# Kernel optimization log

Hardware: AMD Instinct MI355X
Metric: run time of the kernel (lower is better)

The kernel has to match this reference:

```python
import jax, jax.numpy as jnp
import numpy as np

N_STATE = 512
M_IN = 64
P_OUT = 64
BATCH = 32
SEQ = 2048


def setup_inputs() -> dict:
    key = jax.random.key(0)
    k1, k2, k3, k4, k5 = jax.random.split(key, 5)
    u = jax.random.normal(k1, (BATCH, SEQ, M_IN), dtype=jnp.float32)
    # CompanionParam init: a ~ randn * 0.01 (keeps companion matrix stable, near shift matrix)
    a = jax.random.normal(k2, (N_STATE,), dtype=jnp.float32) * 0.01
    B = jax.random.normal(k3, (N_STATE, M_IN), dtype=jnp.float32) * 0.05
    C = jax.random.normal(k4, (P_OUT, N_STATE), dtype=jnp.float32) * 0.05
    D = jax.random.normal(k5, (P_OUT, M_IN), dtype=jnp.float32) * 0.05
    return {"u": u, "a": a, "B": B, "C": C, "D": D}


def companion_matrix(a):
    # A[i+1, i] = 1 on subdiagonal; last column = -flip(a)  (matches CompanionParam.matrix)
    n = a.shape[0]
    idx = jnp.arange(n - 1)
    A = jnp.zeros((n, n), dtype=a.dtype)
    A = A.at[idx + 1, idx].set(1.0)
    A = A.at[:, n - 1].set(-a[::-1])
    return A


def reference(u, a, B, C, D):
    # LTI SSM recurrence: x_t = A x_{t-1} + B u_t ; y_t = C x_t + D u_t
    A = companion_matrix(a)  # (n, n)
    batch, T, m = u.shape
    n = a.shape[0]
    u_t = jnp.transpose(u, (1, 0, 2))  # (T, batch, m)
    Bu = jnp.einsum('tbm,nm->tbn', u_t, B)  # precompute input drive (T, batch, n)

    def step(x, bu):
        x_new = x @ A.T + bu  # (batch, n)
        return x_new, x_new

    x0 = jnp.zeros((batch, n), dtype=u.dtype)
    _, xs = jax.lax.scan(step, x0, Bu)  # xs: (T, batch, n)
    ys = jnp.einsum('tbn,pn->tbp', xs, C) + jnp.einsum('tbm,pm->tbp', u_t, D)
    return jnp.transpose(ys, (1, 0, 2))  # (batch, T, p)
```

## Files before the change

### kernel.cpp

```cpp
#include <hip/hip_runtime.h>

#define SEQ  2048
#define NB   32
#define NS   512
#define MI   64
#define PO   64
#define TB   64
#define NTB  32
#define CH   64
#define NCH  8
#define LDU  72
#define LDD  68
#define SG_LDA 72

typedef __attribute__((ext_vector_type(8))) __bf16 bf16x8;
typedef __attribute__((ext_vector_type(4))) float  floatx4;

__device__ inline unsigned short f2bf(float f) {
    unsigned u = __builtin_bit_cast(unsigned, f);
    u += 0x7fff + ((u >> 16) & 1);
    return (unsigned short)(u >> 16);
}

__global__ void __launch_bounds__(1024) prep_all_kernel(
    const float* __restrict__ u, const float* __restrict__ B,
    const float* __restrict__ C, const float* __restrict__ D,
    const float* __restrict__ a,
    unsigned short* __restrict__ ubf, unsigned short* __restrict__ BflatT,
    unsigned short* __restrict__ Bws, unsigned short* __restrict__ Cws,
    unsigned short* __restrict__ Dws, unsigned short* __restrict__ qT,
    float* __restrict__ hbuf) {
    __shared__ __align__(16) char smem[24576];
    const int bx = blockIdx.x, tid = threadIdx.x;
    if (bx < 512) {
        const size_t base = ((size_t)bx * 1024 + tid) * 8;
        float4 f0 = *(const float4*)(u + base);
        float4 f1 = *(const float4*)(u + base + 4);
        unsigned short tmp[8];
        tmp[0] = f2bf(f0.x); tmp[1] = f2bf(f0.y); tmp[2] = f2bf(f0.z); tmp[3] = f2bf(f0.w);
        tmp[4] = f2bf(f1.x); tmp[5] = f2bf(f1.y); tmp[6] = f2bf(f1.z); tmp[7] = f2bf(f1.w);
        *(uint4*)(ubf + base) = *(uint4*)&tmp[0];
    } else if (bx < 768) {
        const int i = (bx - 512) * 2 + (tid >> 9);
        const int id = tid & 511;
        const int j = id >> 3, q8 = (id & 7) * 8;
        unsigned short tmp[8];
        if (i >= j) {
            const float4 f0 = *(const float4*)(B + (size_t)(i - j) * MI + q8);
            const float4 f1 = *(const float4*)(B + (size_t)(i - j) * MI + q8 + 4);
            tmp[0] = f2bf(f0.x); tmp[1] = f2bf(f0.y); tmp[2] = f2bf(f0.z); tmp[3] = f2bf(f0.w);
            tmp[4] = f2bf(f1.x); tmp[5] = f2bf(f1.y); tmp[6] = f2bf(f1.z); tmp[7] = f2bf(f1.w);
        } else {
#pragma unroll
            for (int z = 0; z < 8; ++z) tmp[z] = 0;
        }
        *(uint4*)(BflatT + (size_t)i * 4096 + j * 64 + q8) = *(uint4*)&tmp[0];
    } else if (bx < 800) {
        float* a_ext = (float*)smem;
        const int p = (bx - 768) * 2 + (tid >> 9);
        const int j0 = tid & 511;
        a_ext[tid] = (tid < NS) ? a[tid] : 0.f;
        __syncthreads();
        float acc0 = 0.f;
        const float4* crow = (const float4*)(C + (size_t)p * NS);
        for (int i4 = 0; i4 < NS / 4; ++i4) {
            const float4 cv = crow[i4];
            const int base = 511 - i4 * 4;
            acc0 += cv.x * a_ext[base + j0]     + cv.y * a_ext[base - 1 + j0] +
                    cv.z * a_ext[base - 2 + j0] + cv.w * a_ext[base - 3 + j0];
        }
        qT[(size_t)p * NS + j0] = f2bf(acc0);
    } else if (bx < 868) {
        const int idx = (bx - 800) * 1024 + tid;
        const int nB = NS * MI, nC = PO * NS, nD = PO * MI;
        if (idx < nB) Bws[idx] = f2bf(B[idx]);
        else if (idx < nB + nC) Cws[idx - nB] = f2bf(C[idx - nB]);
        else if (idx < nB + nC + nD) Dws[idx - nB - nC] = f2bf(D[idx - nB - nC]);
    } else {
        float* a_l     = (float*)smem;
        float* h_ext   = (float*)(smem + 2560);
        float* part    = (float*)(smem + 12800);
        float* rhs_ext = (float*)(smem + 20992);
        const int kk = tid & 63, grp = tid >> 6;

        for (int x = tid; x < 640; x += 1024) a_l[x] = (x < NS) ? a[x] : 0.f;
        for (int x = tid; x < 640; x += 1024) h_ext[x] = 0.f;
        if (tid < 256) rhs_ext[tid] = 0.f;
        __syncthreads();

        float aw[34];
#pragma unroll
        for (int i = 0; i < 34; ++i) aw[i] = a_l[2 * kk + grp * 32 + i];

        if (tid < 64) {
            if (tid == 0) h_ext[512] = 1.f;
            float acc = (tid >= 1) ? a_l[tid - 1] : 0.f;
            for (int s = 1; s < 64; ++s) {
                const float hs = -__shfl(acc, s);
                if (tid == s) h_ext[512 + s] = hs;
                const float av = a_l[(tid > s) ? (tid - 1 - s) : 0];
                acc += (tid > s) ? av * hs : 0.f;
            }
        }
        __syncthreads();

        int t0 = 64;
        while (t0 < SEQ) {
            float acc0 = 0.f, acc1 = 0.f;
#pragma unroll
            for (int m = 0; m < 8; ++m) {
                const float4 hv = *(const float4*)&h_ext[512 + t0 - grp * 32 - 4 - 4 * m];
                acc0 += aw[4 * m + 0] * hv.w + aw[4 * m + 1] * hv.z +
                        aw[4 * m + 2] * hv.y + aw[4 * m + 3] * hv.x;
                acc1 += aw[4 * m + 1] * hv.w + aw[4 * m + 2] * hv.z +
                        aw[4 * m + 3] * hv.y + aw[4 * m + 4] * hv.x;
            }
            *(float2*)&part[grp * 128 + 2 * kk] = make_float2(acc0, acc1);
            __syncthreads();
            if (tid < 128) {
                float r = 0.f;
#pragma unroll
                for (int g = 0; g < 16; ++g) r += part[g * 128 + tid];
                rhs_ext[128 + tid] = -r;
            }
            __syncthreads();
            {
                const int g = tid >> 7, out = tid & 127;
                const int k0 = g * 16;
                float s = 0.f;
#pragma unroll
                for (int k4 = 0; k4 < 4; ++k4) {
                    const float4 h4 = *(const float4*)&h_ext[512 + k0 + 4 * k4];
                    const int base = 128 + out - k0 - 4 * k4;
                    s += h4.x * rhs_ext[base]     + h4.y * rhs_ext[base - 1] +
                         h4.z * rhs_ext[base - 2] + h4.w * rhs_ext[base - 3];
                }
                part[g * 128 + out] = s;
            }
            __syncthreads();
            if (tid < 128) {
                float r = 0.f;
#pragma unroll
                for (int g = 0; g < 8; ++g) r += part[g * 128 + tid];
                h_ext[512 + t0 + tid] = r;
            }
            __syncthreads();
            t0 += (t0 == 64) ? 64 : 128;
        }
        for (int i = tid; i < SEQ; i += 1024) hbuf[i] = h_ext[512 + i];
    }
}

__global__ void __launch_bounds__(256) sgemm_kernel(const unsigned short* __restrict__ ubf,
                                                    const unsigned short* __restrict__ BflatT,
                                                    float* __restrict__ Sbuf) {
    __shared__ unsigned short A_l[2][4 * 64 * SG_LDA];
    __shared__ unsigned short U_l[2][4 * 32 * SG_LDA];
    const int ib = blockIdx.x, b = blockIdx.y;
    const int tid = threadIdx.x, lane = tid & 63, w = tid >> 6;
    const int row16 = lane & 15, quad = lane >> 4;
    const int i0 = ib * 64;
    floatx4 acc[2];
#pragma unroll
    for (int ns = 0; ns < 2; ++ns) acc[ns] = (floatx4){0.f, 0.f, 0.f, 0.f};

    auto stage = [&](int jg, int buf) {
#pragma unroll
        for (int r = 0; r < 8; ++r) {
            const int id = tid + r * 256;
            const int row = id >> 5;
            const int jj = (id >> 3) & 3, q8 = (id & 7) * 8;
            const int j = jg * 4 + jj;
            *(uint4*)&A_l[buf][(jj * 64 + row) * SG_LDA + q8] =
                *(const uint4*)(BflatT + (size_t)(i0 + row) * 4096 + j * 64 + q8);
        }
#pragma unroll
        for (int r = 0; r < 4; ++r) {
            const int id = tid + r * 256;
            const int n = id >> 5;
            const int jj = (id >> 3) & 3, q8 = (id & 7) * 8;
            const int j = jg * 4 + jj;
            *(uint4*)&U_l[buf][(jj * 32 + n) * SG_LDA + q8] =
                *(const uint4*)(ubf + ((size_t)b * SEQ + n * 64 + 63 - j) * MI + q8);
        }
    };

    stage(0, 0);
    __syncthreads();
    for (int jg = 0; jg < 16; ++jg) {
        const int cur = jg & 1;
        if (jg + 1 < 16) stage(jg + 1, cur ^ 1);
#pragma unroll
        for (int jj = 0; jj < 4; ++jj) {
#pragma unroll
            for (int mk = 0; mk < 2; ++mk) {
                const bf16x8 av = *(const bf16x8*)
                    &A_l[cur][(jj * 64 + w * 16 + row16) * SG_LDA + mk * 32 + quad * 8];
#pragma unroll
                for (int ns = 0; ns < 2; ++ns) {
                    const bf16x8 bv = *(const bf16x8*)
                        &U_l[cur][(jj * 32 + ns * 16 + row16) * SG_LDA + mk * 32 + quad * 8];
                    acc[ns] = __builtin_amdgcn_mfma_f32_16x16x32_bf16(av, bv, acc[ns], 0, 0, 0);
                }
            }
        }
        __syncthreads();
    }
#pragma unroll
    for (int ns = 0; ns < 2; ++ns) {
        const int n = ns * 16 + row16;
        float* dst = Sbuf + ((size_t)b * NTB + n) * NS + i0 + w * 16 + quad * 4;
        *(floatx4*)dst = acc[ns];
    }
}

__global__ void __launch_bounds__(256, 4) ytile_kernel(
    const unsigned short* __restrict__ ubf, const unsigned short* __restrict__ Bws,
    const unsigned short* __restrict__ Cws, const unsigned short* __restrict__ Dws,
    const float* __restrict__ Sbuf, float* __restrict__ fbuf, float* __restrict__ y) {
    __shared__ __align__(16) float buDiag[TB * LDD];
    __shared__ __align__(16) unsigned short Gb[TB * LDU];
    __shared__ float seedL[NS];

    const int blk = blockIdx.x, b = blockIdx.y;
    const int t0 = blk * TB;
    const int tid = threadIdx.x;
    const int lane = tid & 63, w = tid >> 6;
    const int row16 = lane & 15, quad = lane >> 4;

    const int dd = lane >> 2, seg = lane & 3;
    const int d  = w * 16 + dd;
    const int tsplit = 63 - d, gseg = tsplit >> 4, jsplit = tsplit & 15;
    const int qb = lane & 60;

    {
        const int mtop = (blk - 1 < 7) ? (blk - 1) : 7;
#pragma unroll
        for (int half = 0; half < 2; ++half) {
            const int s = tid + half * 256;
            const int i = s - 1, q = i >> 6, r = i & 63;
            const int mmax = (mtop < q) ? mtop : q;
            float sd = 0.f;
#pragma unroll
            for (int m = 0; m < 8; ++m) {
                const bool ok = (m <= mmax);
                long off = ((long)b * NTB + (blk - 1 - m)) * NS + (q - m) * 64 + r;
                off = (off < 0) ? 0 : off;
                const float v = Sbuf[off];
                sd += ok ? v : 0.f;
            }
            seedL[s] = sd;
        }
    }

    float cB = 0.f;

    floatx4 accY[4];
#pragma unroll
    for (int nt = 0; nt < 4; ++nt) accY[nt] = (floatx4){0.f, 0.f, 0.f, 0.f};

    bf16x8 ufr0[4], ufr1[4];
#pragma unroll
    for (int nt = 0; nt < 4; ++nt) {
        const size_t ub = ((size_t)b * SEQ + t0 + nt * 16 + row16) * MI;
        ufr0[nt] = *(const bf16x8*)(ubf + ub + quad * 8);
        ufr1[nt] = *(const bf16x8*)(ubf + ub + 32 + quad * 8);
    }

    for (int ch = 0; ch < NCH; ++ch) {
        const bf16x8 bf0 = *(const bf16x8*)(Bws + (size_t)(ch * CH + w * 16 + row16) * MI + quad * 8);
        const bf16x8 bf1 = *(const bf16x8*)(Bws + (size_t)(ch * CH + w * 16 + row16) * MI + 32 + quad * 8);
        const bf16x8 cf0 = *(const bf16x8*)(Cws + (size_t)(w * 16 + row16) * NS + ch * CH + quad * 8);
        const bf16x8 cf1 = *(const bf16x8*)(Cws + (size_t)(w * 16 + row16) * NS + ch * CH + 32 + quad * 8);

#pragma unroll
        for (int nt = 0; nt < 4; ++nt) {
            floatx4 dacc = {0.f, 0.f, 0.f, 0.f};
            dacc = __builtin_amdgcn_mfma_f32_16x16x32_bf16(bf0, ufr0[nt], dacc, 0, 0, 0);
            dacc = __builtin_amdgcn_mfma_f32_16x16x32_bf16(bf1, ufr1[nt], dacc, 0, 0, 0);
            const int t = nt * 16 + row16;
            const int ibase = w * 16 + quad * 4;
#pragma unroll
            for (int r = 0; r < 4; ++r) {
                const int dscat = (ibase + r - t) & 63;
                buDiag[dscat * LDD + t] = dacc[r];
            }
        }
        __syncthreads();

        {
            const float sA = seedL[ch * CH + d];
            const float* rowp = &buDiag[d * LDD + seg * 16];
            const float4 v0 = *(const float4*)(rowp + 0);
            const float4 v1 = *(const float4*)(rowp + 4);
            const float4 v2 = *(const float4*)(rowp + 8);
            const float4 v3 = *(const float4*)(rowp + 12);
            float pv[16];
            pv[0]  = v0.x;          pv[1]  = pv[0]  + v0.y;
            pv[2]  = pv[1]  + v0.z; pv[3]  = pv[2]  + v0.w;
            pv[4]  = pv[3]  + v1.x; pv[5]  = pv[4]  + v1.y;
            pv[6]  = pv[5]  + v1.z; pv[7]  = pv[6]  + v1.w;
            pv[8]  = pv[7]  + v2.x; pv[9]  = pv[8]  + v2.y;
            pv[10] = pv[9]  + v2.z; pv[11] = pv[10] + v2.w;
            pv[12] = pv[11] + v3.x; pv[13] = pv[12] + v3.y;
            pv[14] = pv[13] + v3.z; pv[15] = pv[14] + v3.w;
            const float total = pv[15];
            const float tq0 = __shfl(total, qb + 0);
            const float tq1 = __shfl(total, qb + 1);
            const float tq2 = __shfl(total, qb + 2);
            const float off = (seg > 0 ? tq0 : 0.f) + (seg > 1 ? tq1 : 0.f) +
                              (seg > 2 ? tq2 : 0.f);
            float plocal = pv[0];
#pragma unroll
            for (int j = 1; j < 16; ++j) plocal = (j == jsplit) ? pv[j] : plocal;
            const float Ps = __shfl(off + plocal, qb + gseg);
            const float exitv = sA + Ps;
            const float baseLo = sA, baseHi = cB - Ps;
#pragma unroll
            for (int j = 0; j < 16; ++j) {
                const int t = seg * 16 + j;
                const float outv = ((t <= tsplit) ? baseLo : baseHi) + off + pv[j];
                Gb[t * LDU + ((d + t) & 63)] = f2bf(outv);
            }
            if (ch == NCH - 1) {
                if (seg == 0) fbuf[(size_t)b * SEQ + t0 + tsplit] = exitv;
            }
            cB = exitv;
        }
        __syncthreads();

#pragma unroll
        for (int nt = 0; nt < 4; ++nt) {
            const int t = nt * 16 + row16;
            bf16x8 g0 = *(const bf16x8*)&Gb[t * LDU + quad * 8];
            bf16x8 g1 = *(const bf16x8*)&Gb[t * LDU + 32 + quad * 8];
            accY[nt] = __builtin_amdgcn_mfma_f32_16x16x32_bf16(cf0, g0, accY[nt], 0, 0, 0);
            accY[nt] = __builtin_amdgcn_mfma_f32_16x16x32_bf16(cf1, g1, accY[nt], 0, 0, 0);
        }
    }

    const bf16x8 df0 = *(const bf16x8*)(Dws + (size_t)(w * 16 + row16) * MI + quad * 8);
    const bf16x8 df1 = *(const bf16x8*)(Dws + (size_t)(w * 16 + row16) * MI + 32 + quad * 8);
#pragma unroll
    for (int nt = 0; nt < 4; ++nt) {
        const int t = nt * 16 + row16;
        accY[nt] = __builtin_amdgcn_mfma_f32_16x16x32_bf16(df0, ufr0[nt], accY[nt], 0, 0, 0);
        accY[nt] = __builtin_amdgcn_mfma_f32_16x16x32_bf16(df1, ufr1[nt], accY[nt], 0, 0, 0);
        const int p0 = w * 16 + quad * 4;
        *(floatx4*)(y + ((size_t)b * SEQ + t0 + t) * PO + p0) = accY[nt];
    }
}

__global__ void __launch_bounds__(256) sconv_kernel(const float* __restrict__ fbuf,
                                                    const float* __restrict__ hbuf,
                                                    unsigned short* __restrict__ sbuf) {
    __shared__ __align__(16) float f_l[64 + SEQ];
    __shared__ __align__(16) float h_lc[SEQ + 8];
    __shared__ __align__(16) float part[16][TB];
    const int blk = blockIdx.x, b = blockIdx.y, tid = threadIdx.x;
    const int t0 = blk * TB;
    const int len = t0 + TB;
    {
        const float4* fs = (const float4*)(fbuf + (size_t)b * SEQ);
        const float4* hs = (const float4*)hbuf;
        float4* f4 = (float4*)f_l;
        float4* h4p = (float4*)h_lc;
        if (tid < 16) f4[tid] = make_float4(0.f, 0.f, 0.f, 0.f);
        for (int i = tid; i < len / 4; i += 256) f4[16 + i] = fs[i];
        const int nh4 = len / 4 + 2;
        for (int i = tid; i < nh4; i += 256)
            h4p[i] = (i < SEQ / 4) ? hs[i] : make_float4(0.f, 0.f, 0.f, 0.f);
    }
    __syncthreads();
    const int o4 = (tid & 15) * 4, grp = tid >> 4;
    const int tb4 = t0 + o4;
    float a0 = 0.f, a1 = 0.f, a2 = 0.f, a3 = 0.f;
    for (int j4 = grp * 4; j4 <= tb4 + 3; j4 += 64) {
        const float4 hv = *(const float4*)&h_lc[j4];
        const int A = tb4 - j4;
        const float4 q0 = *(const float4*)&f_l[60 + A];
        const float4 q1 = *(const float4*)&f_l[64 + A];
        a0 += hv.x * q1.x + hv.y * q0.w + hv.z * q0.z + hv.w * q0.y;
        a1 += hv.x * q1.y + hv.y * q1.x + hv.z * q0.w + hv.w * q0.z;
        a2 += hv.x * q1.z + hv.y * q1.y + hv.z * q1.x + hv.w * q0.w;
        a3 += hv.x * q1.w + hv.y * q1.z + hv.z * q1.y + hv.w * q1.x;
    }
    *(float4*)&part[grp][o4] = make_float4(a0, a1, a2, a3);
    __syncthreads();
    if (tid < TB) {
        float r = 0.f;
#pragma unroll
        for (int g = 0; g < 16; ++g) r += part[g][tid];
        sbuf[(size_t)b * SEQ + t0 + tid] = f2bf(r);
    }
}

__global__ void __launch_bounds__(256) corr_kernel(
    const unsigned short* __restrict__ sbuf, const unsigned short* __restrict__ qT,
    float* __restrict__ y) {
    __shared__ unsigned short s_bf[NS + TB];
    __shared__ unsigned short Sw[2][TB * LDU];
    const int blk = blockIdx.x, b = blockIdx.y, tid = threadIdx.x;
    const int t0 = blk * TB;
    const int lane = tid & 63, w = tid >> 6;
    const int row16 = lane & 15, quad = lane >> 4;
    for (int idx = tid; idx < NS + TB; idx += 256) {
        const int t = t0 - NS + idx;
        s_bf[idx] = (t >= 0) ? sbuf[(size_t)b * SEQ + t] : (unsigned short)0;
    }
    floatx4 acc[4];
#pragma unroll
    for (int nt = 0; nt < 4; ++nt) acc[nt] = (floatx4){0.f, 0.f, 0.f, 0.f};
    __syncthreads();

    for (int ch = 0; ch < NCH; ++ch) {
        const int buf = ch & 1;
        const bf16x8 qf0 = *(const bf16x8*)(qT + (size_t)(w * 16 + row16) * NS + ch * CH + quad * 8);
        const bf16x8 qf1 = *(const bf16x8*)(qT + (size_t)(w * 16 + row16) * NS + ch * CH + 32 + quad * 8);
        {
            const int r = tid >> 2, c0 = (tid & 3) * 16;
            unsigned short tmp[16];
            const int base = 511 + r - ch * CH - c0;
#pragma unroll
            for (int jj = 0; jj < 16; ++jj) tmp[jj] = s_bf[base - jj];
            *(uint4*)&Sw[buf][r * LDU + c0]     = *(uint4*)&tmp[0];
            *(uint4*)&Sw[buf][r * LDU + c0 + 8] = *(uint4*)&tmp[8];
        }
        __syncthreads();
#pragma unroll
        for (int nt = 0; nt < 4; ++nt) {
            const int t = nt * 16 + row16;
            bf16x8 s0 = *(const bf16x8*)&Sw[buf][t * LDU + quad * 8];
            bf16x8 s1 = *(const bf16x8*)&Sw[buf][t * LDU + 32 + quad * 8];
            acc[nt] = __builtin_amdgcn_mfma_f32_16x16x32_bf16(qf0, s0, acc[nt], 0, 0, 0);
            acc[nt] = __builtin_amdgcn_mfma_f32_16x16x32_bf16(qf1, s1, acc[nt], 0, 0, 0);
        }
    }
#pragma unroll
    for (int nt = 0; nt < 4; ++nt) {
        const int t = nt * 16 + row16;
        const int p0 = w * 16 + quad * 4;
        float* yp = y + ((size_t)b * SEQ + t0 + t) * PO + p0;
        floatx4 old = *(const floatx4*)yp;
        *(floatx4*)yp = old - acc[nt];
    }
}

extern "C" void kernel_launch(void* const* d_in, const int* in_sizes, int n_in,
                              void* d_out, int out_size, void* d_ws,
                              size_t ws_size, hipStream_t stream) {
    const float* u  = (const float*)d_in[0];
    const float* a  = (const float*)d_in[1];
    const float* B  = (const float*)d_in[2];
    const float* Cm = (const float*)d_in[3];
    const float* Dm = (const float*)d_in[4];
    float* y = (float*)d_out;

    char* ws = (char*)d_ws;
    unsigned short* Bws = (unsigned short*)ws;                  ws += NS * MI * 2;
    unsigned short* Cws = (unsigned short*)ws;                  ws += PO * NS * 2;
    unsigned short* Dws = (unsigned short*)ws;                  ws += PO * MI * 2;
    unsigned short* qTw = (unsigned short*)ws;                  ws += PO * NS * 2;
    unsigned short* ubf = (unsigned short*)ws;                  ws += (size_t)NB * SEQ * MI * 2;
    unsigned short* Bft = (unsigned short*)ws;                  ws += (size_t)NS * 4096 * 2;
    float* Sbuf = (float*)ws;                                   ws += (size_t)NB * NTB * NS * 4;
    float* fbuf = (float*)ws;                                   ws += (size_t)NB * SEQ * 4;
    unsigned short* sbuf = (unsigned short*)ws;                 ws += (size_t)NB * SEQ * 4;
    float* hbuf = (float*)ws;

    prep_all_kernel<<<dim3(869), dim3(1024), 0, stream>>>(
        u, B, Cm, Dm, a, ubf, Bft, Bws, Cws, Dws, qTw, hbuf);
    sgemm_kernel<<<dim3(8, 32), dim3(256), 0, stream>>>(ubf, Bft, Sbuf);
    ytile_kernel<<<dim3(NTB, NB), dim3(256), 0, stream>>>(
        ubf, Bws, Cws, Dws, Sbuf, fbuf, y);
    sconv_kernel<<<dim3(NTB, NB), dim3(256), 0, stream>>>(fbuf, hbuf, sbuf);
    corr_kernel<<<dim3(NTB, NB), dim3(256), 0, stream>>>(sbuf, qTw, y);
}
```

Before: 193.3 us.

## Double-buffer Gb and software-pipeline B/C loads across chunks in ytile kernel

Restructures the ytile chunk loop so the Bu MFMA scatter for the next chunk runs right after the current chunk's output MFMAs. Gb is double-buffered so the next scan pass can write while the previous one is read, and B/C fragments for chunk ch+1 are prefetched early. The seed accumulation now uses a conditional load instead of a clamped, always-executed load. Each chunk still needs two barriers, and register pressure may rise from the prefetched fragments.

```diff
diff --git a/kernel.cpp b/kernel.cpp
--- a/kernel.cpp
+++ b/kernel.cpp
@@ -219,7 +219,7 @@
     const unsigned short* __restrict__ Cws, const unsigned short* __restrict__ Dws,
     const float* __restrict__ Sbuf, float* __restrict__ fbuf, float* __restrict__ y) {
     __shared__ __align__(16) float buDiag[TB * LDD];
-    __shared__ __align__(16) unsigned short Gb[TB * LDU];
+    __shared__ __align__(16) unsigned short Gb[2][TB * LDU];
     __shared__ float seedL[NS];
 
     const int blk = blockIdx.x, b = blockIdx.y;
@@ -243,11 +243,8 @@
             float sd = 0.f;
 #pragma unroll
             for (int m = 0; m < 8; ++m) {
-                const bool ok = (m <= mmax);
-                long off = ((long)b * NTB + (blk - 1 - m)) * NS + (q - m) * 64 + r;
-                off = (off < 0) ? 0 : off;
-                const float v = Sbuf[off];
-                sd += ok ? v : 0.f;
+                if (m <= mmax)
+                    sd += Sbuf[((size_t)b * NTB + (blk - 1 - m)) * NS + (q - m) * 64 + r];
             }
             seedL[s] = sd;
         }
@@ -267,17 +264,15 @@
         ufr1[nt] = *(const bf16x8*)(ubf + ub + 32 + quad * 8);
     }
 
-    for (int ch = 0; ch < NCH; ++ch) {
-        const bf16x8 bf0 = *(const bf16x8*)(Bws + (size_t)(ch * CH + w * 16 + row16) * MI + quad * 8);
-        const bf16x8 bf1 = *(const bf16x8*)(Bws + (size_t)(ch * CH + w * 16 + row16) * MI + 32 + quad * 8);
-        const bf16x8 cf0 = *(const bf16x8*)(Cws + (size_t)(w * 16 + row16) * NS + ch * CH + quad * 8);
-        const bf16x8 cf1 = *(const bf16x8*)(Cws + (size_t)(w * 16 + row16) * NS + ch * CH + 32 + quad * 8);
-
+    const size_t bRow = (size_t)(w * 16 + row16) * MI;
+    const size_t cRow = (size_t)(w * 16 + row16) * NS;
+
+    auto phaseA = [&](const bf16x8 pb0, const bf16x8 pb1) {
 #pragma unroll
         for (int nt = 0; nt < 4; ++nt) {
             floatx4 dacc = {0.f, 0.f, 0.f, 0.f};
-            dacc = __builtin_amdgcn_mfma_f32_16x16x32_bf16(bf0, ufr0[nt], dacc, 0, 0, 0);
-            dacc = __builtin_amdgcn_mfma_f32_16x16x32_bf16(bf1, ufr1[nt], dacc, 0, 0, 0);
+            dacc = __builtin_amdgcn_mfma_f32_16x16x32_bf16(pb0, ufr0[nt], dacc, 0, 0, 0);
+            dacc = __builtin_amdgcn_mfma_f32_16x16x32_bf16(pb1, ufr1[nt], dacc, 0, 0, 0);
             const int t = nt * 16 + row16;
             const int ibase = w * 16 + quad * 4;
 #pragma unroll
@@ -286,8 +281,19 @@
                 buDiag[dscat * LDD + t] = dacc[r];
             }
         }
-        __syncthreads();
-
+    };
+
+    bf16x8 cf0, cf1;
+    {
+        const bf16x8 b0 = *(const bf16x8*)(Bws + bRow + quad * 8);
+        const bf16x8 b1 = *(const bf16x8*)(Bws + bRow + 32 + quad * 8);
+        cf0 = *(const bf16x8*)(Cws + cRow + quad * 8);
+        cf1 = *(const bf16x8*)(Cws + cRow + 32 + quad * 8);
+        phaseA(b0, b1);
+    }
+    __syncthreads();
+
+    for (int ch = 0; ch < NCH; ++ch) {
         {
             const float sA = seedL[ch * CH + d];
             const float* rowp = &buDiag[d * LDD + seg * 16];
@@ -320,7 +326,7 @@
             for (int j = 0; j < 16; ++j) {
                 const int t = seg * 16 + j;
                 const float outv = ((t <= tsplit) ? baseLo : baseHi) + off + pv[j];
-                Gb[t * LDU + ((d + t) & 63)] = f2bf(outv);
+                Gb[ch & 1][t * LDU + ((d + t) & 63)] = f2bf(outv);
             }
             if (ch == NCH - 1) {
                 if (seg == 0) fbuf[(size_t)b * SEQ + t0 + tsplit] = exitv;
@@ -329,13 +335,27 @@
         }
         __syncthreads();
 
+        bf16x8 nbf0, nbf1, ncf0 = cf0, ncf1 = cf1;
+        const bool more = (ch + 1 < NCH);
+        if (more) {
+            const size_t bOff = (size_t)((ch + 1) * CH) * MI + bRow;
+            nbf0 = *(const bf16x8*)(Bws + bOff + quad * 8);
+            nbf1 = *(const bf16x8*)(Bws + bOff + 32 + quad * 8);
+            ncf0 = *(const bf16x8*)(Cws + cRow + (ch + 1) * CH + quad * 8);
+            ncf1 = *(const bf16x8*)(Cws + cRow + (ch + 1) * CH + 32 + quad * 8);
+        }
 #pragma unroll
         for (int nt = 0; nt < 4; ++nt) {
             const int t = nt * 16 + row16;
-            bf16x8 g0 = *(const bf16x8*)&Gb[t * LDU + quad * 8];
-            bf16x8 g1 = *(const bf16x8*)&Gb[t * LDU + 32 + quad * 8];
+            bf16x8 g0 = *(const bf16x8*)&Gb[ch & 1][t * LDU + quad * 8];
+            bf16x8 g1 = *(const bf16x8*)&Gb[ch & 1][t * LDU + 32 + quad * 8];
             accY[nt] = __builtin_amdgcn_mfma_f32_16x16x32_bf16(cf0, g0, accY[nt], 0, 0, 0);
             accY[nt] = __builtin_amdgcn_mfma_f32_16x16x32_bf16(cf1, g1, accY[nt], 0, 0, 0);
+        }
+        if (more) {
+            phaseA(nbf0, nbf1);
+            cf0 = ncf0; cf1 = ncf1;
+            __syncthreads();
         }
     }
 
```

Measured after the change: 202.3 us. +4.7%, slower.
